# Kernel tuning notes

Measured on AMD Instinct MI355X. Metric: run time of the kernel, lower is better.

The kernel has to match this reference:

```python
import jax, jax.numpy as jnp
import numpy as np

N, E, DIM, HID, TEMB = 50000, 600000, 128, 128, 8
IN_DIM = 3 * DIM + TEMB  # zi, zj, |zi-zj|, type_emb


def setup_inputs() -> dict:
    key = jax.random.key(0)
    ks = jax.random.split(key, 16)
    s = lambda *sh: 1.0 / np.sqrt(sh[-1])
    return {
        "z": jax.random.normal(ks[0], (N, DIM), jnp.float32),
        "edge_index": jax.random.randint(ks[1], (2, E), 0, N, jnp.int64),
        "edge_type": jax.random.randint(ks[2], (E,), 0, 2, jnp.int64),
        "type_emb": jax.random.normal(ks[3], (2, TEMB), jnp.float32),
        "ew1": jax.random.normal(ks[4], (HID, IN_DIM), jnp.float32) * s(HID, IN_DIM),
        "eb1": jnp.zeros((HID,), jnp.float32),
        "ew2": jax.random.normal(ks[5], (1, HID), jnp.float32) * s(1, HID),
        "eb2": jnp.zeros((1,), jnp.float32),
        "mw1": jax.random.normal(ks[6], (DIM, DIM), jnp.float32) * s(DIM, DIM),
        "mb1": jnp.zeros((DIM,), jnp.float32),
        "mw2": jax.random.normal(ks[7], (DIM, DIM), jnp.float32) * s(DIM, DIM),
        "mb2": jnp.zeros((DIM,), jnp.float32),
        "gamma": jnp.ones((DIM,), jnp.float32),
        "beta": jnp.zeros((DIM,), jnp.float32),
    }


def reference(z, edge_index, edge_type, type_emb, ew1, eb1, ew2, eb2,
              mw1, mb1, mw2, mb2, gamma, beta):
    src, dst = edge_index[0], edge_index[1]
    zi = z[src]          # [E, DIM]
    zj = z[dst]          # [E, DIM]
    te = type_emb[edge_type]  # [E, TEMB]
    e_in = jnp.concatenate([zi, zj, jnp.abs(zi - zj), te], axis=1)  # [E, IN_DIM]

    # edge MLP -> scalar weight per edge, sigmoid squashed
    h = jax.nn.relu(e_in @ ew1.T + eb1)
    w = jax.nn.sigmoid((h @ ew2.T + eb2)[:, 0])  # [E]

    n = z.shape[0]
    # numerically-stable segment softmax over edges grouped by src
    max_per_src = jnp.full((n,), -1e9, dtype=z.dtype).at[src].max(w)
    w_exp = jnp.exp(w - max_per_src[src])
    sum_per_src = jax.ops.segment_sum(w_exp, src, num_segments=n)
    alpha = w_exp / (sum_per_src[src] + 1e-12)  # [E]

    # message MLP on destination features, weighted by alpha
    msg = (jax.nn.relu(zj @ mw1.T + mb1) @ mw2.T + mb2) * alpha[:, None]  # [E, DIM]
    agg = jax.ops.segment_sum(msg, src, num_segments=n)  # [N, DIM]

    # residual + LayerNorm (dropout is identity in eval mode)
    x = z + agg
    mu = jnp.mean(x, axis=-1, keepdims=True)
    var = jnp.mean(jnp.square(x - mu), axis=-1, keepdims=True)
    out = (x - mu) * jax.lax.rsqrt(var + 1e-5) * gamma + beta
    return (out, alpha)
```

## Files before the change

### kernel.cpp

```cpp
#include <hip/hip_runtime.h>
#include <math.h>

constexpr int NN  = 50000;
constexpr int NE  = 600000;
constexpr int D   = 128;
constexpr int IND = 392;

typedef __attribute__((ext_vector_type(8))) short bf16x8;
typedef __attribute__((ext_vector_type(4))) float f32x4;

__device__ __forceinline__ float4 ld4(const float* p) { return *reinterpret_cast<const float4*>(p); }

__device__ __forceinline__ unsigned short f2bf(float f) {
  unsigned int u = __float_as_uint(f);
  u += 0x7fffu + ((u >> 16) & 1u);
  return (unsigned short)(u >> 16);
}
__device__ __forceinline__ float bf2f(unsigned short s) {
  return __uint_as_float(((unsigned int)s) << 16);
}

__global__ __launch_bounds__(256) void k_preph(
    const float* __restrict__ ew1, const float* __restrict__ type_emb,
    const float* __restrict__ mw1, const float* __restrict__ mw2,
    const int* __restrict__ ei,
    unsigned short* __restrict__ Wab, unsigned short* __restrict__ Wbb,
    unsigned short* __restrict__ Wcb,
    unsigned short* __restrict__ m1h, unsigned short* __restrict__ m1l,
    unsigned short* __restrict__ m2h, unsigned short* __restrict__ m2l,
    float* __restrict__ tvg, int* __restrict__ deg)
{
  const int b = blockIdx.x, t = threadIdx.x;
  if (b < 64) {
    int g = b * 256 + t;
    int o = g >> 7, k = g & 127;
    Wab[g] = f2bf(ew1[o * IND + k]);
    Wbb[g] = f2bf(ew1[o * IND + 128 + k]);
    Wcb[g] = f2bf(ew1[o * IND + 256 + k]);
    float w1 = mw1[g];
    unsigned short h1 = f2bf(w1);
    m1h[g] = h1; m1l[g] = f2bf(w1 - bf2f(h1));
    float w2 = mw2[g];
    unsigned short h2 = f2bf(w2);
    m2h[g] = h2; m2l[g] = f2bf(w2 - bf2f(h2));
    if (b == 0) {
      int oo = t & 127, ty = t >> 7;
      float s = 0.f;
#pragma unroll
      for (int j = 0; j < 8; ++j) s += ew1[oo * IND + 384 + j] * type_emb[ty * 8 + j];
      tvg[ty * 128 + oo] = s;
    }
  } else {
    int e = (b - 64) * 256 + t;
    if (e < NE) atomicAdd(&deg[ei[e]], 1);
  }
}

template <int TERMS>
__device__ __forceinline__ void mm_acc(
    const unsigned short (*Xh)[136], const unsigned short (*Xl)[136],
    const unsigned short (*Wh)[136], const unsigned short (*Wl)[136],
    int me, int r, int q, f32x4 acc[8])
{
#pragma unroll
  for (int ks = 0; ks < 4; ++ks) {
    bf16x8 ah = *reinterpret_cast<const bf16x8*>(&Xh[me + r][ks * 32 + q * 8]);
    bf16x8 al;
    if (TERMS >= 2) al = *reinterpret_cast<const bf16x8*>(&Xl[me + r][ks * 32 + q * 8]);
#pragma unroll
    for (int nt = 0; nt < 8; ++nt) {
      bf16x8 bh = *reinterpret_cast<const bf16x8*>(&Wh[nt * 16 + r][ks * 32 + q * 8]);
      acc[nt] = __builtin_amdgcn_mfma_f32_16x16x32_bf16(ah, bh, acc[nt], 0, 0, 0);
      if (TERMS >= 2)
        acc[nt] = __builtin_amdgcn_mfma_f32_16x16x32_bf16(al, bh, acc[nt], 0, 0, 0);
      if (TERMS == 3) {
        bf16x8 bl = *reinterpret_cast<const bf16x8*>(&Wl[nt * 16 + r][ks * 32 + q * 8]);
        acc[nt] = __builtin_amdgcn_mfma_f32_16x16x32_bf16(ah, bl, acc[nt], 0, 0, 0);
      }
    }
  }
}

__global__ __launch_bounds__(512, 1) void k_node_mfma(
    const float* __restrict__ z,
    const unsigned short* __restrict__ Wab, const unsigned short* __restrict__ Wbb,
    const unsigned short* __restrict__ m1h, const unsigned short* __restrict__ m1l,
    const unsigned short* __restrict__ m2h, const unsigned short* __restrict__ m2l,
    const float* __restrict__ mb1, const float* __restrict__ mb2,
    unsigned short* __restrict__ Ab, unsigned short* __restrict__ Bb,
    unsigned short* __restrict__ Mb, unsigned short* __restrict__ zb)
{
  __shared__ unsigned short Xh[128][136], Xl[128][136];
  __shared__ unsigned short Wh[128][136], Wl[128][136];
  const int t  = threadIdx.x;
  const int n0 = blockIdx.x * 128;

#pragma unroll
  for (int it = 0; it < 8; ++it) {
    int f = it * 512 + t, rr = f >> 5, c4 = (f & 31) * 4;
    int n = n0 + rr; if (n >= NN) n = NN - 1;
    float4 v = ld4(&z[(size_t)n * D + c4]);
    ushort4 hi, lo;
    hi.x = f2bf(v.x); lo.x = f2bf(v.x - bf2f(hi.x));
    hi.y = f2bf(v.y); lo.y = f2bf(v.y - bf2f(hi.y));
    hi.z = f2bf(v.z); lo.z = f2bf(v.z - bf2f(hi.z));
    hi.w = f2bf(v.w); lo.w = f2bf(v.w - bf2f(hi.w));
    *reinterpret_cast<ushort4*>(&Xh[rr][c4]) = hi;
    *reinterpret_cast<ushort4*>(&Xl[rr][c4]) = lo;
    if (n0 + rr < NN)
      *reinterpret_cast<ushort4*>(&zb[(size_t)(n0 + rr) * D + c4]) = hi;
  }
#pragma unroll
  for (int it = 0; it < 4; ++it) {
    int f = it * 512 + t, row = f >> 4, c8 = (f & 15) * 8;
    *reinterpret_cast<bf16x8*>(&Wh[row][c8]) =
        *reinterpret_cast<const bf16x8*>(&Wab[row * 128 + c8]);
  }
  __syncthreads();

  const int l = t & 63, q = l >> 4, r = l & 15;
  const int me = (t >> 6) * 16;

  f32x4 acc[8];

#pragma unroll
  for (int nt = 0; nt < 8; ++nt) acc[nt] = (f32x4){0.f, 0.f, 0.f, 0.f};
  mm_acc<1>(Xh, Xl, Wh, Wl, me, r, q, acc);
#pragma unroll
  for (int nt = 0; nt < 8; ++nt)
#pragma unroll
    for (int i = 0; i < 4; ++i) {
      int n = n0 + me + q * 4 + i;
      if (n < NN) Ab[(size_t)n * D + nt * 16 + r] = f2bf(acc[nt][i]);
    }
  __syncthreads();

#pragma unroll
  for (int it = 0; it < 4; ++it) {
    int f = it * 512 + t, row = f >> 4, c8 = (f & 15) * 8;
    *reinterpret_cast<bf16x8*>(&Wh[row][c8]) =
        *reinterpret_cast<const bf16x8*>(&Wbb[row * 128 + c8]);
  }
  __syncthreads();
#pragma unroll
  for (int nt = 0; nt < 8; ++nt) acc[nt] = (f32x4){0.f, 0.f, 0.f, 0.f};
  mm_acc<1>(Xh, Xl, Wh, Wl, me, r, q, acc);
#pragma unroll
  for (int nt = 0; nt < 8; ++nt)
#pragma unroll
    for (int i = 0; i < 4; ++i) {
      int n = n0 + me + q * 4 + i;
      if (n < NN) Bb[(size_t)n * D + nt * 16 + r] = f2bf(acc[nt][i]);
    }
  __syncthreads();

#pragma unroll
  for (int it = 0; it < 4; ++it) {
    int f = it * 512 + t, row = f >> 4, c8 = (f & 15) * 8;
    *reinterpret_cast<bf16x8*>(&Wh[row][c8]) =
        *reinterpret_cast<const bf16x8*>(&m1h[row * 128 + c8]);
    *reinterpret_cast<bf16x8*>(&Wl[row][c8]) =
        *reinterpret_cast<const bf16x8*>(&m1l[row * 128 + c8]);
  }
  __syncthreads();
#pragma unroll
  for (int nt = 0; nt < 8; ++nt) acc[nt] = (f32x4){0.f, 0.f, 0.f, 0.f};
  mm_acc<3>(Xh, Xl, Wh, Wl, me, r, q, acc);
#pragma unroll
  for (int nt = 0; nt < 8; ++nt) {
    int col = nt * 16 + r;
    float b1 = mb1[col];
#pragma unroll
    for (int i = 0; i < 4; ++i) {
      float h = fmaxf(acc[nt][i] + b1, 0.0f);
      unsigned short hh = f2bf(h);
      Xh[me + q * 4 + i][col] = hh;
      Xl[me + q * 4 + i][col] = f2bf(h - bf2f(hh));
    }
  }
  __syncthreads();

#pragma unroll
  for (int it = 0; it < 4; ++it) {
    int f = it * 512 + t, row = f >> 4, c8 = (f & 15) * 8;
    *reinterpret_cast<bf16x8*>(&Wh[row][c8]) =
        *reinterpret_cast<const bf16x8*>(&m2h[row * 128 + c8]);
    *reinterpret_cast<bf16x8*>(&Wl[row][c8]) =
        *reinterpret_cast<const bf16x8*>(&m2l[row * 128 + c8]);
  }
  __syncthreads();
#pragma unroll
  for (int nt = 0; nt < 8; ++nt) acc[nt] = (f32x4){0.f, 0.f, 0.f, 0.f};
  mm_acc<3>(Xh, Xl, Wh, Wl, me, r, q, acc);
#pragma unroll
  for (int nt = 0; nt < 8; ++nt) {
    int col = nt * 16 + r;
    float b2 = mb2[col];
#pragma unroll
    for (int i = 0; i < 4; ++i) {
      int n = n0 + me + q * 4 + i;
      if (n < NN) Mb[(size_t)n * D + col] = f2bf(acc[nt][i] + b2);
    }
  }
}

constexpr int SNB = 196;

__global__ __launch_bounds__(256) void k_scan1(const int* __restrict__ deg,
                                               int* __restrict__ pre,
                                               int* __restrict__ bsum)
{
  __shared__ int ps[256];
  const int t = threadIdx.x, b = blockIdx.x;
  const int i = b * 256 + t;
  int v = (i < NN) ? deg[i] : 0;
  ps[t] = v;
  __syncthreads();
  for (int off = 1; off < 256; off <<= 1) {
    int u = (t >= off) ? ps[t - off] : 0;
    __syncthreads();
    ps[t] += u;
    __syncthreads();
  }
  pre[i] = ps[t] - v;
  if (t == 255) bsum[b] = ps[255];
}

__global__ __launch_bounds__(256) void k_scan2(const int* __restrict__ bsum,
                                               int* __restrict__ bbase)
{
  __shared__ int ps[256];
  const int t = threadIdx.x;
  int v = (t < SNB) ? bsum[t] : 0;
  ps[t] = v;
  __syncthreads();
  for (int off = 1; off < 256; off <<= 1) {
    int u = (t >= off) ? ps[t - off] : 0;
    __syncthreads();
    ps[t] += u;
    __syncthreads();
  }
  if (t < SNB) bbase[t] = ps[t] - v;
}

__global__ __launch_bounds__(256) void k_scan3(const int* __restrict__ pre,
                                               const int* __restrict__ bbase,
                                               int* __restrict__ rowptr,
                                               int* __restrict__ cursor)
{
  const int t = threadIdx.x, b = blockIdx.x;
  const int i = b * 256 + t;
  if (i < NN) {
    int v = pre[i] + bbase[b];
    rowptr[i] = v;
    cursor[i] = v;
  }
  if (i == 0) rowptr[NN] = NE;
}

__global__ __launch_bounds__(256) void k_fill(const int* __restrict__ ei,
                                              int* __restrict__ cursor,
                                              int* __restrict__ eid,
                                              int* __restrict__ de_perm,
                                              int* __restrict__ inv)
{
  int e = blockIdx.x * 256 + threadIdx.x;
  if (e < NE) {
    int pos = atomicAdd(&cursor[ei[e]], 1);
    eid[pos] = e;
    de_perm[pos] = ei[NE + e];
    inv[e] = pos;
  }
}

__global__ __launch_bounds__(512, 6) void k_edge_mfma(
    const unsigned short* __restrict__ zb, const int* __restrict__ ei,
    const int* __restrict__ etype,
    const unsigned short* __restrict__ Wcb, const float* __restrict__ tvg,
    const float* __restrict__ eb1, const float* __restrict__ ew2,
    const float* __restrict__ eb2,
    const unsigned short* __restrict__ Ab, const unsigned short* __restrict__ Bb,
    const int* __restrict__ eid, const int* __restrict__ de_perm,
    float* __restrict__ wexp_perm)
{
  __shared__ unsigned short Xb[128 * 128];
  __shared__ unsigned short Wb[64 * 128];
  __shared__ unsigned short se[128], de[128];
  __shared__ unsigned char  tyg[128];

  const int t = threadIdx.x;
  const int nx = gridDim.x >> 3;
  const int sb = (blockIdx.x & 7) * nx + (blockIdx.x >> 3);
  const int e0 = sb * 128;

  if (t < 128) {
    int pos = e0 + t;
    if (pos < NE) {
      int e  = eid[pos];
      se[t]  = (unsigned short)ei[e];
      de[t]  = (unsigned short)de_perm[pos];
      tyg[t] = (unsigned char)etype[e];
    } else { se[t] = 0; de[t] = 0; tyg[t] = 0; }
  }
#pragma unroll
  for (int it = 0; it < 2; ++it) {
    int f = it * 512 + t, row = f >> 4, c = f & 15;
    int a = (row * 256 + c * 16) ^ ((row & 7) << 4);
    *reinterpret_cast<bf16x8*>((char*)Wb + a) =
        *reinterpret_cast<const bf16x8*>(&Wcb[row * 128 + c * 8]);
  }
  __syncthreads();

#pragma unroll
  for (int it = 0; it < 8; ++it) {
    int f = it * 512 + t, r = f >> 5, c4 = f & 31;
    ushort4 a4 = *reinterpret_cast<const ushort4*>(&zb[(size_t)se[r] * D + c4 * 4]);
    ushort4 b4 = *reinterpret_cast<const ushort4*>(&zb[(size_t)de[r] * D + c4 * 4]);
    ushort4 v;
    v.x = f2bf(fabsf(bf2f(a4.x) - bf2f(b4.x)));
    v.y = f2bf(fabsf(bf2f(a4.y) - bf2f(b4.y)));
    v.z = f2bf(fabsf(bf2f(a4.z) - bf2f(b4.z)));
    v.w = f2bf(fabsf(bf2f(a4.w) - bf2f(b4.w)));
    int a = (r * 256 + c4 * 8) ^ ((r & 7) << 4);
    *reinterpret_cast<ushort4*>((char*)Xb + a) = v;
  }
  __syncthreads();

  const int l = t & 63, q = l >> 4, r = l & 15;
  const int me = (t >> 6) * 16;

  f32x4 acc[8];
#pragma unroll
  for (int nt = 0; nt < 8; ++nt) acc[nt] = (f32x4){0.f, 0.f, 0.f, 0.f};

#pragma unroll
  for (int ks = 0; ks < 4; ++ks) {
    int xa = ((me + r) * 256 + ks * 64 + q * 16) ^ ((r & 7) << 4);
    bf16x8 a = *reinterpret_cast<const bf16x8*>((const char*)Xb + xa);
#pragma unroll
    for (int ntl = 0; ntl < 4; ++ntl) {
      int wrow = ntl * 16 + r;
      int wa = (wrow * 256 + ks * 64 + q * 16) ^ ((wrow & 7) << 4);
      bf16x8 b = *reinterpret_cast<const bf16x8*>((const char*)Wb + wa);
      acc[ntl] = __builtin_amdgcn_mfma_f32_16x16x32_bf16(a, b, acc[ntl], 0, 0, 0);
    }
  }
  __syncthreads();

#pragma unroll
  for (int it = 0; it < 2; ++it) {
    int f = it * 512 + t, row = f >> 4, c = f & 15;
    int a = (row * 256 + c * 16) ^ ((row & 7) << 4);
    *reinterpret_cast<bf16x8*>((char*)Wb + a) =
        *reinterpret_cast<const bf16x8*>(&Wcb[(64 + row) * 128 + c * 8]);
  }
  __syncthreads();

#pragma unroll
  for (int ks = 0; ks < 4; ++ks) {
    int xa = ((me + r) * 256 + ks * 64 + q * 16) ^ ((r & 7) << 4);
    bf16x8 a = *reinterpret_cast<const bf16x8*>((const char*)Xb + xa);
#pragma unroll
    for (int ntl = 0; ntl < 4; ++ntl) {
      int wrow = ntl * 16 + r;
      int wa = (wrow * 256 + ks * 64 + q * 16) ^ ((wrow & 7) << 4);
      bf16x8 b = *reinterpret_cast<const bf16x8*>((const char*)Wb + wa);
      acc[4 + ntl] = __builtin_amdgcn_mfma_f32_16x16x32_bf16(a, b, acc[4 + ntl], 0, 0, 0);
    }
  }

  int s[4], dd[4], ty[4];
#pragma unroll
  for (int i = 0; i < 4; ++i) {
    int el = me + q * 4 + i;
    s[i] = se[el]; dd[i] = de[el]; ty[i] = tyg[el];
  }
  float p[4] = {0.f, 0.f, 0.f, 0.f};
#pragma unroll
  for (int nt = 0; nt < 8; ++nt) {
    int col = nt * 16 + r;
    float e1  = eb1[col], w2 = ew2[col];
    float tva = tvg[col], tvb = tvg[128 + col];
#pragma unroll
    for (int i = 0; i < 4; ++i) {
      float h = acc[nt][i] + bf2f(Ab[(size_t)s[i] * D + col])
              + bf2f(Bb[(size_t)dd[i] * D + col]) + (ty[i] ? tvb : tva) + e1;
      p[i] += fmaxf(h, 0.f) * w2;
    }
  }
#pragma unroll
  for (int m = 1; m < 16; m <<= 1) {
#pragma unroll
    for (int i = 0; i < 4; ++i) p[i] += __shfl_xor(p[i], m);
  }
  if (r == 0) {
    float b2 = eb2[0];
#pragma unroll
    for (int i = 0; i < 4; ++i) {
      int pos = e0 + me + q * 4 + i;
      if (pos < NE) {
        float w = 1.0f / (1.0f + expf(-(p[i] + b2)));
        wexp_perm[pos] = expf(w);
      }
    }
  }
}

__global__ __launch_bounds__(256) void k_agg(
    const float* __restrict__ z, const float* __restrict__ wexp_perm,
    const unsigned short* __restrict__ Mb, const int* __restrict__ rowptr,
    const int* __restrict__ de_perm,
    const float* __restrict__ gamma, const float* __restrict__ beta,
    float* __restrict__ out, float* __restrict__ sumw)
{
  const int t = threadIdx.x;
  const int n = blockIdx.x * 4 + (t >> 6);
  const int l = t & 63;
  const int start = rowptr[n], end = rowptr[n + 1];

  float tot = 0.f;
  for (int base = start; base < end; base += 64) {
    if (base + l < end) tot += wexp_perm[base + l];
  }
#pragma unroll
  for (int off = 32; off; off >>= 1) tot += __shfl_xor(tot, off);
  if (l == 0) sumw[n] = tot;
  const float inv = 1.0f / (tot + 1e-12f);

  float2 acc = make_float2(0.f, 0.f);
  for (int base = start; base < end; base += 64) {
    int cnt = min(64, end - base);
    int dd = 0;
    float al = 0.f;
    if (l < cnt) {
      int pos = base + l;
      al = wexp_perm[pos] * inv;
      dd = de_perm[pos];
    }
    int i = 0;
    for (; i + 4 <= cnt; i += 4) {
      float a0 = __shfl(al, i),     a1 = __shfl(al, i + 1);
      float a2 = __shfl(al, i + 2), a3 = __shfl(al, i + 3);
      int   d0 = __shfl(dd, i),     d1 = __shfl(dd, i + 1);
      int   d2 = __shfl(dd, i + 2), d3 = __shfl(dd, i + 3);
      ushort2 m0 = *reinterpret_cast<const ushort2*>(&Mb[(size_t)d0 * D + l * 2]);
      ushort2 m1 = *reinterpret_cast<const ushort2*>(&Mb[(size_t)d1 * D + l * 2]);
      ushort2 m2 = *reinterpret_cast<const ushort2*>(&Mb[(size_t)d2 * D + l * 2]);
      ushort2 m3 = *reinterpret_cast<const ushort2*>(&Mb[(size_t)d3 * D + l * 2]);
      acc.x = fmaf(a0, bf2f(m0.x), acc.x); acc.y = fmaf(a0, bf2f(m0.y), acc.y);
      acc.x = fmaf(a1, bf2f(m1.x), acc.x); acc.y = fmaf(a1, bf2f(m1.y), acc.y);
      acc.x = fmaf(a2, bf2f(m2.x), acc.x); acc.y = fmaf(a2, bf2f(m2.y), acc.y);
      acc.x = fmaf(a3, bf2f(m3.x), acc.x); acc.y = fmaf(a3, bf2f(m3.y), acc.y);
    }
    for (; i < cnt; ++i) {
      float a = __shfl(al, i);
      int   d = __shfl(dd, i);
      ushort2 m = *reinterpret_cast<const ushort2*>(&Mb[(size_t)d * D + l * 2]);
      acc.x = fmaf(a, bf2f(m.x), acc.x);
      acc.y = fmaf(a, bf2f(m.y), acc.y);
    }
  }

  float2 xz = *reinterpret_cast<const float2*>(&z[(size_t)n * D + l * 2]);
  float x0 = xz.x + acc.x, x1 = xz.y + acc.y;
  float s = x0 + x1;
#pragma unroll
  for (int off = 32; off; off >>= 1) s += __shfl_xor(s, off);
  const float mu = s * (1.0f / 128.0f);
  float d0 = x0 - mu, d1 = x1 - mu;
  float q = d0 * d0 + d1 * d1;
#pragma unroll
  for (int off = 32; off; off >>= 1) q += __shfl_xor(q, off);
  const float rstd = rsqrtf(q * (1.0f / 128.0f) + 1e-5f);
  float2 g = *reinterpret_cast<const float2*>(&gamma[l * 2]);
  float2 b = *reinterpret_cast<const float2*>(&beta[l * 2]);
  float2 o = make_float2(d0 * rstd * g.x + b.x, d1 * rstd * g.y + b.y);
  *reinterpret_cast<float2*>(&out[(size_t)n * D + l * 2]) = o;
}

__global__ __launch_bounds__(256) void k_alpha(
    const int* __restrict__ ei, const int* __restrict__ inv,
    const float* __restrict__ wexp_perm, const float* __restrict__ sumw,
    float* __restrict__ alpha_out)
{
  int e = blockIdx.x * 256 + threadIdx.x;
  if (e < NE) {
    float we = wexp_perm[inv[e]];
    float sm = sumw[ei[e]];
    alpha_out[e] = we / (sm + 1e-12f);
  }
}

extern "C" void kernel_launch(void* const* d_in, const int* in_sizes, int n_in,
                              void* d_out, int out_size, void* d_ws, size_t ws_size,
                              hipStream_t stream)
{
  const float* z        = (const float*)d_in[0];
  const int*   ei       = (const int*)d_in[1];
  const int*   etype    = (const int*)d_in[2];
  const float* type_emb = (const float*)d_in[3];
  const float* ew1      = (const float*)d_in[4];
  const float* eb1      = (const float*)d_in[5];
  const float* ew2      = (const float*)d_in[6];
  const float* eb2      = (const float*)d_in[7];
  const float* mw1      = (const float*)d_in[8];
  const float* mb1      = (const float*)d_in[9];
  const float* mw2      = (const float*)d_in[10];
  const float* mb2      = (const float*)d_in[11];
  const float* gamma    = (const float*)d_in[12];
  const float* beta     = (const float*)d_in[13];

  float*          ws        = (float*)d_ws;
  unsigned short* Ab        = (unsigned short*)(ws);
  unsigned short* Bb        = (unsigned short*)(ws + 3200000);
  unsigned short* Mb        = (unsigned short*)(ws + 6400000);
  unsigned short* zb        = (unsigned short*)(ws + 9600000);
  float*          wexp_perm = ws + 12800000;
  int*            deg       = (int*)(ws + 13400000);
  int*            rowptr    = deg + 50000;
  int*            cursor    = rowptr + 50004;
  int*            eid       = cursor + 50000;
  int*            de_perm   = eid + 600000;
  unsigned short* Wcb       = (unsigned short*)(ws + 14800000);
  float*          tvg       = ws + 14810000;
  unsigned short* Wab       = (unsigned short*)(ws + 14820000);
  unsigned short* Wbb       = (unsigned short*)(ws + 14830000);
  unsigned short* m1h       = (unsigned short*)(ws + 14840000);
  unsigned short* m1l       = (unsigned short*)(ws + 14850000);
  unsigned short* m2h       = (unsigned short*)(ws + 14860000);
  unsigned short* m2l       = (unsigned short*)(ws + 14870000);
  int*            pre       = (int*)(ws + 14880000);
  int*            bsum      = (int*)(ws + 14940000);
  int*            bbase     = (int*)(ws + 14941000);
  int*            inv       = (int*)(ws + 15000000);
  float*          sumw      = ws + 15700000;

  float* out       = (float*)d_out;
  float* alpha_out = out + (size_t)NN * D;

  hipMemsetAsync(deg, 0, 50000 * sizeof(int), stream);

  k_preph<<<64 + (NE + 255) / 256, 256, 0, stream>>>(
      ew1, type_emb, mw1, mw2, ei,
      Wab, Wbb, Wcb, m1h, m1l, m2h, m2l, tvg, deg);
  k_scan1<<<SNB, 256, 0, stream>>>(deg, pre, bsum);
  k_scan2<<<1, 256, 0, stream>>>(bsum, bbase);
  k_scan3<<<SNB, 256, 0, stream>>>(pre, bbase, rowptr, cursor);
  k_fill<<<(NE + 255) / 256, 256, 0, stream>>>(ei, cursor, eid, de_perm, inv);
  k_node_mfma<<<(NN + 127) / 128, 512, 0, stream>>>(z, Wab, Wbb, m1h, m1l,
                                                    m2h, m2l, mb1, mb2,
                                                    Ab, Bb, Mb, zb);
  k_edge_mfma<<<(NE + 127) / 128, 512, 0, stream>>>(zb, ei, etype, Wcb, tvg,
                                                    eb1, ew2, eb2, Ab, Bb,
                                                    eid, de_perm, wexp_perm);
  k_agg<<<NN / 4, 256, 0, stream>>>(z, wexp_perm, Mb, rowptr, de_perm,
                                    gamma, beta, out, sumw);
  k_alpha<<<(NE + 255) / 256, 256, 0, stream>>>(ei, inv, wexp_perm, sumw,
                                                alpha_out);
}
```

Before: 247.4 us.

## Transpose MFMA operands for vectorized gathers and fuse node-side weight loads

In the edge kernel, the MFMA operand order is swapped so each lane holds four consecutive hidden columns of a single edge rather than one column across four edges. The per-edge gathers of Ab/Bb rows and the bias, type and weight vectors can then be done as ushort4/float4 vector loads, and the cross-lane reduction shrinks from 4 shuffle steps per value to 2. In the node pre-pass, both Wab and Wbb are loaded into shared memory at once, reusing the Wl buffer, which removes two barriers and one reload phase. The risk is that passing (Wl, Wh) into mm_acc as hi/lo reuses the template in a way that must still match the intended single-precision path.

```diff
diff --git a/kernel.cpp b/kernel.cpp
--- a/kernel.cpp
+++ b/kernel.cpp
@@ -115,6 +115,8 @@
     int f = it * 512 + t, row = f >> 4, c8 = (f & 15) * 8;
     *reinterpret_cast<bf16x8*>(&Wh[row][c8]) =
         *reinterpret_cast<const bf16x8*>(&Wab[row * 128 + c8]);
+    *reinterpret_cast<bf16x8*>(&Wl[row][c8]) =
+        *reinterpret_cast<const bf16x8*>(&Wbb[row * 128 + c8]);
   }
   __syncthreads();
 
@@ -133,18 +135,10 @@
       int n = n0 + me + q * 4 + i;
       if (n < NN) Ab[(size_t)n * D + nt * 16 + r] = f2bf(acc[nt][i]);
     }
-  __syncthreads();
-
-#pragma unroll
-  for (int it = 0; it < 4; ++it) {
-    int f = it * 512 + t, row = f >> 4, c8 = (f & 15) * 8;
-    *reinterpret_cast<bf16x8*>(&Wh[row][c8]) =
-        *reinterpret_cast<const bf16x8*>(&Wbb[row * 128 + c8]);
-  }
-  __syncthreads();
+
 #pragma unroll
   for (int nt = 0; nt < 8; ++nt) acc[nt] = (f32x4){0.f, 0.f, 0.f, 0.f};
-  mm_acc<1>(Xh, Xl, Wh, Wl, me, r, q, acc);
+  mm_acc<1>(Xh, Xl, Wl, Wh, me, r, q, acc);
 #pragma unroll
   for (int nt = 0; nt < 8; ++nt)
 #pragma unroll
@@ -336,13 +330,13 @@
 #pragma unroll
   for (int ks = 0; ks < 4; ++ks) {
     int xa = ((me + r) * 256 + ks * 64 + q * 16) ^ ((r & 7) << 4);
-    bf16x8 a = *reinterpret_cast<const bf16x8*>((const char*)Xb + xa);
+    bf16x8 x = *reinterpret_cast<const bf16x8*>((const char*)Xb + xa);
 #pragma unroll
     for (int ntl = 0; ntl < 4; ++ntl) {
       int wrow = ntl * 16 + r;
       int wa = (wrow * 256 + ks * 64 + q * 16) ^ ((wrow & 7) << 4);
-      bf16x8 b = *reinterpret_cast<const bf16x8*>((const char*)Wb + wa);
-      acc[ntl] = __builtin_amdgcn_mfma_f32_16x16x32_bf16(a, b, acc[ntl], 0, 0, 0);
+      bf16x8 w = *reinterpret_cast<const bf16x8*>((const char*)Wb + wa);
+      acc[ntl] = __builtin_amdgcn_mfma_f32_16x16x32_bf16(w, x, acc[ntl], 0, 0, 0);
     }
   }
   __syncthreads();
@@ -359,49 +353,41 @@
 #pragma unroll
   for (int ks = 0; ks < 4; ++ks) {
     int xa = ((me + r) * 256 + ks * 64 + q * 16) ^ ((r & 7) << 4);
-    bf16x8 a = *reinterpret_cast<const bf16x8*>((const char*)Xb + xa);
+    bf16x8 x = *reinterpret_cast<const bf16x8*>((const char*)Xb + xa);
 #pragma unroll
     for (int ntl = 0; ntl < 4; ++ntl) {
       int wrow = ntl * 16 + r;
       int wa = (wrow * 256 + ks * 64 + q * 16) ^ ((wrow & 7) << 4);
-      bf16x8 b = *reinterpret_cast<const bf16x8*>((const char*)Wb + wa);
-      acc[4 + ntl] = __builtin_amdgcn_mfma_f32_16x16x32_bf16(a, b, acc[4 + ntl], 0, 0, 0);
-    }
-  }
-
-  int s[4], dd[4], ty[4];
-#pragma unroll
-  for (int i = 0; i < 4; ++i) {
-    int el = me + q * 4 + i;
-    s[i] = se[el]; dd[i] = de[el]; ty[i] = tyg[el];
-  }
-  float p[4] = {0.f, 0.f, 0.f, 0.f};
+      bf16x8 w = *reinterpret_cast<const bf16x8*>((const char*)Wb + wa);
+      acc[4 + ntl] = __builtin_amdgcn_mfma_f32_16x16x32_bf16(w, x, acc[4 + ntl], 0, 0, 0);
+    }
+  }
+
+  const int el = me + r;
+  const int s  = se[el], dd = de[el];
+  const float* tvp = tvg + (tyg[el] ? 128 : 0);
+  float p = 0.f;
 #pragma unroll
   for (int nt = 0; nt < 8; ++nt) {
-    int col = nt * 16 + r;
-    float e1  = eb1[col], w2 = ew2[col];
-    float tva = tvg[col], tvb = tvg[128 + col];
-#pragma unroll
-    for (int i = 0; i < 4; ++i) {
-      float h = acc[nt][i] + bf2f(Ab[(size_t)s[i] * D + col])
-              + bf2f(Bb[(size_t)dd[i] * D + col]) + (ty[i] ? tvb : tva) + e1;
-      p[i] += fmaxf(h, 0.f) * w2;
-    }
-  }
-#pragma unroll
-  for (int m = 1; m < 16; m <<= 1) {
-#pragma unroll
-    for (int i = 0; i < 4; ++i) p[i] += __shfl_xor(p[i], m);
-  }
-  if (r == 0) {
-    float b2 = eb2[0];
-#pragma unroll
-    for (int i = 0; i < 4; ++i) {
-      int pos = e0 + me + q * 4 + i;
-      if (pos < NE) {
-        float w = 1.0f / (1.0f + expf(-(p[i] + b2)));
-        wexp_perm[pos] = expf(w);
-      }
+    int c0 = nt * 16 + q * 4;
+    ushort4 a4 = *reinterpret_cast<const ushort4*>(&Ab[(size_t)s  * D + c0]);
+    ushort4 b4 = *reinterpret_cast<const ushort4*>(&Bb[(size_t)dd * D + c0]);
+    float4 tv = ld4(&tvp[c0]);
+    float4 e1 = ld4(&eb1[c0]);
+    float4 w2 = ld4(&ew2[c0]);
+    float h;
+    h = acc[nt][0] + bf2f(a4.x) + bf2f(b4.x) + tv.x + e1.x; p += fmaxf(h, 0.f) * w2.x;
+    h = acc[nt][1] + bf2f(a4.y) + bf2f(b4.y) + tv.y + e1.y; p += fmaxf(h, 0.f) * w2.y;
+    h = acc[nt][2] + bf2f(a4.z) + bf2f(b4.z) + tv.z + e1.z; p += fmaxf(h, 0.f) * w2.z;
+    h = acc[nt][3] + bf2f(a4.w) + bf2f(b4.w) + tv.w + e1.w; p += fmaxf(h, 0.f) * w2.w;
+  }
+  p += __shfl_xor(p, 16);
+  p += __shfl_xor(p, 32);
+  if (q == 0) {
+    int pos = e0 + el;
+    if (pos < NE) {
+      float w = 1.0f / (1.0f + expf(-(p + eb2[0])));
+      wexp_perm[pos] = expf(w);
     }
   }
 }
```

After: 292.9 us. 1.18x slower.
